# Optimization experiments

Hardware: AMD Instinct MI355X
Metric: run time of the kernel (lower is better)

Reference implementation:

```python
import jax, jax.numpy as jnp
import numpy as np

B, S, H = 4, 2048, 768
NUM_POS = B * (S // 4)  # fixed count of positive clc_label entries (2048, even)
NEG_BIG = -1000000000.0


def setup_inputs() -> dict:
    key = jax.random.key(0)
    k1, k2, k3, k4, k5 = jax.random.split(key, 5)
    encoded_states = jax.random.normal(k1, (B, S, H), dtype=jnp.float32)
    # sorted cell-ids -> contiguous segments for the equality mask
    indicator = jnp.sort(jax.random.randint(k2, (B, S), 0, 256, dtype=jnp.int32), axis=-1)
    # clc_label: first S//4 positions per row are positive targets (class ids in [1,S)),
    # last S//2 positions are -1 (attendable keys), rest 0 (ignored)
    pos_labels = jax.random.randint(k3, (B, S // 4), 1, S, dtype=jnp.int32)
    clc_label = jnp.zeros((B, S), dtype=jnp.int32)
    clc_label = clc_label.at[:, : S // 4].set(pos_labels)
    clc_label = clc_label.at[:, S // 2:].set(-1)
    # uniform_linear params (torch Linear: y = x @ W.T + b)
    W = jax.random.normal(k4, (H, H), dtype=jnp.float32) / np.sqrt(H)
    b = jax.random.normal(k5, (H,), dtype=jnp.float32) * 0.01
    return {"encoded_states": encoded_states, "W": W, "b": b,
            "indicator": indicator, "clc_label": clc_label}


def _ce(logits, labels):
    # mean cross entropy; all labels are > 0 here so ignore_index=0 never triggers
    logp = jax.nn.log_softmax(logits, axis=-1)
    return -jnp.take_along_axis(logp, labels[:, None], axis=1).mean()


def reference(encoded_states, W, b, indicator, clc_label):
    # indicator-equality mask matmul == within-segment sum (the segment-reduce emulation)
    seg_mask = (indicator[:, :, None] == indicator[:, None, :]).astype(encoded_states.dtype)  # [B,S,S]
    agg = jnp.einsum("bij,bjh->bih", seg_mask, encoded_states)  # [B,S,H]
    # Q and K use the SAME linear on the same input -> compute once
    proj = jnp.tanh(agg @ W.T + b)  # [B,S,H]
    scores = jnp.einsum("bih,bjh->bij", proj, proj)  # [B,S,S]
    # attend only to positions where clc_label < 0
    allow = (clc_label < 0)[:, None, :]  # [B,1,S]
    scores = scores + jnp.where(allow, 0.0, NEG_BIG).astype(scores.dtype)
    flat = scores.reshape(-1, S)          # [B*S, S]
    labels = clc_label.reshape(-1)        # [B*S]
    pos_idx = jnp.nonzero(labels > 0, size=NUM_POS)[0]  # row-major order == torch bool-indexing
    logits = flat[pos_idx]                # [NUM_POS, S]
    labs = labels[pos_idx]                # [NUM_POS]
    sep_logits, sep_labels = logits[0::2], labs[0::2]
    tok_logits, tok_labels = logits[1::2], labs[1::2]
    sep_loss = _ce(sep_logits, sep_labels)
    tok_loss = _ce(tok_logits, tok_labels)
    sep_correct = jnp.sum((jnp.argmax(sep_logits, axis=-1).astype(jnp.int32) == sep_labels).astype(jnp.float32))
    tok_correct = jnp.sum((jnp.argmax(tok_logits, axis=-1).astype(jnp.int32) == tok_labels).astype(jnp.float32))
    sep_count = jnp.asarray(sep_logits.shape[0] + 1e-6, dtype=jnp.float32)
    tok_count = jnp.asarray(tok_logits.shape[0] + 1e-6, dtype=jnp.float32)
    return ((sep_loss, sep_correct, sep_count), (tok_loss, tok_correct, tok_count))
```

## Files before the change

### kernel.cpp

```cpp
#include <hip/hip_runtime.h>
#include <math.h>
#include <limits.h>

#define BB 4
#define SS 2048
#define HH 768
#define MAXSEG 256
#define NUM_POS (BB*(SS/4))
#define NEG_BIG -1000000000.0f

typedef _Float16 f16x8 __attribute__((ext_vector_type(8)));
typedef _Float16 f16x4 __attribute__((ext_vector_type(4)));
typedef float    f32x4 __attribute__((ext_vector_type(4)));

__device__ __forceinline__ int blockExclScan(int v, int* sWave, int lane, int wid)
{
  int x = v;
  #pragma unroll
  for (int off = 1; off < 64; off <<= 1) {
    int y = __shfl_up(x, off, 64);
    if (lane >= off) x += y;
  }
  if (lane == 63) sWave[wid] = x;
  __syncthreads();
  int base = 0;
  for (int w = 0; w < wid; w++) base += sWave[w];
  return base + x - v;
}

__global__ __launch_bounds__(256) void k_scan(
    const int* __restrict__ ind, const int* __restrict__ clc,
    const float* __restrict__ W, _Float16* __restrict__ Wh,
    int* __restrict__ seg_id, int* __restrict__ seg_start,
    int* __restrict__ nseg, int* __restrict__ pos_cnt,
    int* __restrict__ allowCnt, int* __restrict__ firstAllow,
    int* __restrict__ posSegOff, int* __restrict__ posSeg,
    float* __restrict__ accum, int* __restrict__ counter)
{
  int t = threadIdx.x;
  if (blockIdx.x >= BB) {
    int idx = (blockIdx.x - BB)*256 + t;
    float4 v = ((const float4*)W)[idx];
    f16x4 h;
    h[0] = (_Float16)v.x; h[1] = (_Float16)v.y;
    h[2] = (_Float16)v.z; h[3] = (_Float16)v.w;
    *(f16x4*)(Wh + (size_t)idx*4) = h;
    return;
  }
  int b = blockIdx.x;
  int lane = t & 63, wid = t >> 6;
  __shared__ int sInd[SS];
  __shared__ int sWave[4];
  __shared__ int sAC[MAXSEG];
  __shared__ int sFA[MAXSEG];
  if (b == 0 && t < 4) accum[t] = 0.f;
  if (b == 0 && t == 4) *counter = 0;
  for (int i = t; i < SS; i += 256) sInd[i] = ind[b*SS + i];
  sAC[t] = 0; sFA[t] = INT_MAX;
  __syncthreads();

  int i0 = t * 8;
  int f[8], cv[8];
  int lsum = 0;
  #pragma unroll
  for (int u = 0; u < 8; u++) {
    int i = i0 + u;
    f[u] = (i == 0) ? 0 : (sInd[i] != sInd[i-1]);
    cv[u] = clc[b*SS + i];
    lsum += f[u];
  }
  int run = blockExclScan(lsum, sWave, lane, wid);
  int rid[8];
  #pragma unroll
  for (int u = 0; u < 8; u++) {
    int i = i0 + u;
    run += f[u];
    rid[u] = run;
    seg_id[b*SS + i] = run;
    if (f[u] || i == 0) seg_start[b*(MAXSEG+1) + run] = i;
  }
  if (t == 255) { nseg[b] = run + 1; seg_start[b*(MAXSEG+1) + run + 1] = SS; }

  #pragma unroll
  for (int u = 0; u < 8; u++) {
    if (cv[u] < 0) {
      atomicAdd(&sAC[rid[u]], 1);
      atomicMin(&sFA[rid[u]], i0 + u);
    }
  }
  __syncthreads();
  allowCnt[b*MAXSEG + t]   = sAC[t];
  firstAllow[b*MAXSEG + t] = sFA[t];
  __syncthreads();

  int p[8], kk[8];
  int psum = 0;
  #pragma unroll
  for (int u = 0; u < 8; u++) { p[u] = (cv[u] > 0) ? 1 : 0; psum += p[u]; }
  int rank = blockExclScan(psum, sWave, lane, wid);
  #pragma unroll
  for (int u = 0; u < 8; u++) {
    kk[u] = rank;
    if (p[u]) rank++;
  }
  if (t == 255) pos_cnt[b] = rank;
  __syncthreads();

  sAC[t] = 0;
  __syncthreads();
  #pragma unroll
  for (int u = 0; u < 8; u++) if (p[u]) atomicAdd(&sAC[rid[u]], 1);
  __syncthreads();
  int cnt = sAC[t];
  int off = blockExclScan(cnt, sWave, lane, wid);
  posSegOff[b*(MAXSEG+1) + t] = off;
  if (t == 255) posSegOff[b*(MAXSEG+1) + 256] = off + cnt;
  __syncthreads();
  sFA[t] = off;
  __syncthreads();
  #pragma unroll
  for (int u = 0; u < 8; u++) {
    if (p[u]) {
      int pos = atomicAdd(&sFA[rid[u]], 1);
      posSeg[b*SS + pos] = (kk[u] << 16) | (i0 + u);
    }
  }
}

__global__ __launch_bounds__(192) void k_segsum(
    const float* __restrict__ es, const int* __restrict__ seg_start,
    const int* __restrict__ nseg, _Float16* __restrict__ segsum_h)
{
  int blk = blockIdx.x, t = threadIdx.x;
  int b = blk >> 8, s = blk & 255;
  float4 acc = {0.f, 0.f, 0.f, 0.f};
  if (s < nseg[b]) {
    int st = seg_start[b*(MAXSEG+1) + s];
    int en = seg_start[b*(MAXSEG+1) + s + 1];
    const float* basep = es + (size_t)b*SS*HH + t*4;
    for (int i = st; i < en; i++) {
      float4 v = *(const float4*)(basep + (size_t)i*HH);
      acc.x += v.x; acc.y += v.y; acc.z += v.z; acc.w += v.w;
    }
  }
  f16x4 h;
  h[0] = (_Float16)acc.x; h[1] = (_Float16)acc.y;
  h[2] = (_Float16)acc.z; h[3] = (_Float16)acc.w;
  *(f16x4*)(segsum_h + ((size_t)b*MAXSEG + s)*HH + t*4) = h;
}

__global__ __launch_bounds__(256) void k_gemmU(
    const _Float16* __restrict__ Ah, const _Float16* __restrict__ Wh,
    const float* __restrict__ bias, _Float16* __restrict__ Uh)
{
  int tid = threadIdx.x;
  int w = tid >> 6, lane = tid & 63;
  int tile = blockIdx.x*4 + w;
  int tm = tile / 24, tn = tile % 24;
  int rb = tm*32, cb = tn*32;
  int m0 = lane & 15, quad = lane >> 4;
  const _Float16* A0 = Ah + (size_t)(rb + m0)*HH + quad*8;
  const _Float16* A1 = A0 + (size_t)16*HH;
  const _Float16* B0 = Wh + (size_t)(cb + m0)*HH + quad*8;
  const _Float16* B1 = B0 + (size_t)16*HH;
  f32x4 acc00 = {0.f,0.f,0.f,0.f}, acc01 = {0.f,0.f,0.f,0.f};
  f32x4 acc10 = {0.f,0.f,0.f,0.f}, acc11 = {0.f,0.f,0.f,0.f};
  #pragma unroll 4
  for (int k0 = 0; k0 < HH; k0 += 32) {
    f16x8 a0 = *(const f16x8*)(A0 + k0);
    f16x8 a1 = *(const f16x8*)(A1 + k0);
    f16x8 b0 = *(const f16x8*)(B0 + k0);
    f16x8 b1 = *(const f16x8*)(B1 + k0);
    acc00 = __builtin_amdgcn_mfma_f32_16x16x32_f16(a0, b0, acc00, 0, 0, 0);
    acc01 = __builtin_amdgcn_mfma_f32_16x16x32_f16(a0, b1, acc01, 0, 0, 0);
    acc10 = __builtin_amdgcn_mfma_f32_16x16x32_f16(a1, b0, acc10, 0, 0, 0);
    acc11 = __builtin_amdgcn_mfma_f32_16x16x32_f16(a1, b1, acc11, 0, 0, 0);
  }
  float bc0 = bias[cb + m0], bc1 = bias[cb + 16 + m0];
  int r0 = rb + quad*4;
  #pragma unroll
  for (int i = 0; i < 4; i++) {
    Uh[(size_t)(r0+i)*HH    + cb + m0]      = (_Float16)tanhf(acc00[i] + bc0);
    Uh[(size_t)(r0+i)*HH    + cb + 16 + m0] = (_Float16)tanhf(acc01[i] + bc1);
    Uh[(size_t)(r0+16+i)*HH + cb + m0]      = (_Float16)tanhf(acc10[i] + bc0);
    Uh[(size_t)(r0+16+i)*HH + cb + 16 + m0] = (_Float16)tanhf(acc11[i] + bc1);
  }
}

__global__ __launch_bounds__(256) void k_gram(
    const _Float16* __restrict__ Uh, float* __restrict__ G)
{
  int tid = threadIdx.x;
  int w = tid >> 6, lane = tid & 63;
  int tile = blockIdx.x*4 + w;
  int b = tile >> 8, rem = tile & 255;
  int rb = (rem >> 4)*16, cb = (rem & 15)*16;
  int m0 = lane & 15, quad = lane >> 4;
  const _Float16* Ub = Uh + (size_t)b*MAXSEG*HH;
  const _Float16* A0 = Ub + (size_t)(rb + m0)*HH + quad*8;
  const _Float16* B0 = Ub + (size_t)(cb + m0)*HH + quad*8;
  f32x4 acc = {0.f,0.f,0.f,0.f};
  #pragma unroll 4
  for (int k0 = 0; k0 < HH; k0 += 32) {
    f16x8 a  = *(const f16x8*)(A0 + k0);
    f16x8 bb = *(const f16x8*)(B0 + k0);
    acc = __builtin_amdgcn_mfma_f32_16x16x32_f16(a, bb, acc, 0, 0, 0);
  }
  float* Gb = G + (size_t)b*MAXSEG*MAXSEG;
  int r0 = rb + quad*4;
  #pragma unroll
  for (int i = 0; i < 4; i++)
    Gb[(size_t)(r0+i)*MAXSEG + cb + m0] = acc[i];
}

__global__ __launch_bounds__(256) void k_tail(
    const float* __restrict__ G, const int* __restrict__ seg_id,
    const int* __restrict__ clc, const int* __restrict__ nseg,
    const int* __restrict__ pos_cnt, const int* __restrict__ allowCnt,
    const int* __restrict__ firstAllow, const int* __restrict__ posSegOff,
    const int* __restrict__ posSeg,
    float* __restrict__ accum, int* __restrict__ counter,
    float* __restrict__ out)
{
  __shared__ float sP[4][4];
  int t = threadIdx.x;
  int lane = t & 63, wid = t >> 6;
  int row = blockIdx.x * 4 + wid;
  int b = row >> 8, si = row & 255;

  float l0 = 0.f, c0 = 0.f, l1 = 0.f, c1 = 0.f;
  if (si < nseg[b]) {
    const float* g = G + ((size_t)b*MAXSEG + si)*MAXSEG;
    const int* ac = allowCnt + b*MAXSEG;
    const int* fa = firstAllow + b*MAXSEG;
    float gv[4]; int av[4], fv[4];
    #pragma unroll
    for (int q = 0; q < 4; q++) {
      int s = lane + 64*q;
      gv[q] = g[s]; av[q] = ac[s]; fv[q] = fa[s];
    }
    float m = -INFINITY;
    #pragma unroll
    for (int q = 0; q < 4; q++) if (av[q] > 0) m = fmaxf(m, gv[q]);
    #pragma unroll
    for (int off = 32; off > 0; off >>= 1) m = fmaxf(m, __shfl_xor(m, off, 64));
    float s = 0.f;
    #pragma unroll
    for (int q = 0; q < 4; q++) if (av[q] > 0) s += (float)av[q] * expf(gv[q] - m);
    #pragma unroll
    for (int off = 32; off > 0; off >>= 1) s += __shfl_xor(s, off, 64);
    float bv = -INFINITY; int bi = INT_MAX;
    #pragma unroll
    for (int q = 0; q < 4; q++) {
      if (av[q] > 0 && (gv[q] > bv || (gv[q] == bv && fv[q] < bi))) { bv = gv[q]; bi = fv[q]; }
    }
    #pragma unroll
    for (int off = 32; off > 0; off >>= 1) {
      float ov = __shfl_xor(bv, off, 64);
      int   oi = __shfl_xor(bi, off, 64);
      if (ov > bv || (ov == bv && oi < bi)) { bv = ov; bi = oi; }
    }
    float lseV = m + logf(s);

    int base_b = 0;
    for (int bb2 = 0; bb2 < b; bb2++) base_b += pos_cnt[bb2];
    int st = posSegOff[b*(MAXSEG+1) + si];
    int en = posSegOff[b*(MAXSEG+1) + si + 1];
    for (int pp = st + lane; pp < en; pp += 64) {
      int e = posSeg[b*SS + pp];
      int i = e & 0xFFFF, k = e >> 16;
      int L = clc[b*SS + i];
      int sL = seg_id[b*SS + L];
      float vL = G[((size_t)b*MAXSEG + si)*MAXSEG + sL]
               + (clc[b*SS + L] < 0 ? 0.0f : NEG_BIG);
      float loss = lseV - vL;
      float corr = (bi == L) ? 1.0f : 0.0f;
      if ((base_b + k) & 1) { l1 += loss; c1 += corr; }
      else                  { l0 += loss; c0 += corr; }
    }
  }
  #pragma unroll
  for (int off = 32; off > 0; off >>= 1) {
    l0 += __shfl_down(l0, off, 64);
    c0 += __shfl_down(c0, off, 64);
    l1 += __shfl_down(l1, off, 64);
    c1 += __shfl_down(c1, off, 64);
  }
  if (lane == 0) { sP[wid][0] = l0; sP[wid][1] = c0; sP[wid][2] = l1; sP[wid][3] = c1; }
  __syncthreads();
  if (t == 0) {
    float v0 = sP[0][0]+sP[1][0]+sP[2][0]+sP[3][0];
    float v1 = sP[0][1]+sP[1][1]+sP[2][1]+sP[3][1];
    float v2 = sP[0][2]+sP[1][2]+sP[2][2]+sP[3][2];
    float v3 = sP[0][3]+sP[1][3]+sP[2][3]+sP[3][3];
    atomicAdd(&accum[0], v0);
    atomicAdd(&accum[1], v1);
    atomicAdd(&accum[2], v2);
    atomicAdd(&accum[3], v3);
    __threadfence();
    int old = atomicAdd(counter, 1);
    if (old == gridDim.x - 1) {
      float L0 = atomicAdd(&accum[0], 0.0f);
      float C0 = atomicAdd(&accum[1], 0.0f);
      float L1 = atomicAdd(&accum[2], 0.0f);
      float C1 = atomicAdd(&accum[3], 0.0f);
      float n = (float)(NUM_POS/2);
      out[0] = L0 / n;
      out[1] = C0;
      out[2] = n + 1e-6f;
      out[3] = L1 / n;
      out[4] = C1;
      out[5] = n + 1e-6f;
    }
  }
}

extern "C" void kernel_launch(void* const* d_in, const int* in_sizes, int n_in,
                              void* d_out, int out_size, void* d_ws, size_t ws_size,
                              hipStream_t stream)
{
  const float* es   = (const float*)d_in[0];
  const float* W    = (const float*)d_in[1];
  const float* bias = (const float*)d_in[2];
  const int*   ind  = (const int*)d_in[3];
  const int*   clc  = (const int*)d_in[4];
  float* out = (float*)d_out;

  char* ws = (char*)d_ws;
  float* accum      = (float*)(ws + 0);
  int*   counter    = (int*)(ws + 16);
  int*   nseg       = (int*)(ws + 256);
  int*   pos_cnt    = (int*)(ws + 512);
  int*   seg_start  = (int*)(ws + 1024);
  int*   seg_id     = (int*)(ws + 8192);
  int*   posSegOff  = (int*)(ws + 40960);
  int*   posSeg     = (int*)(ws + 49152);
  int*   allowCnt   = (int*)(ws + 81920);
  int*   firstAllow = (int*)(ws + 86016);
  _Float16* segsum_h = (_Float16*)(ws + 90112);
  _Float16* Wh       = (_Float16*)(ws + 1662976);
  _Float16* Uh       = (_Float16*)(ws + 2842624);
  float*    G        = (float*)(ws + 4415488);

  k_scan<<<BB + 576, 256, 0, stream>>>(ind, clc, W, Wh, seg_id, seg_start,
                                       nseg, pos_cnt, allowCnt, firstAllow,
                                       posSegOff, posSeg, accum, counter);
  k_segsum<<<BB*MAXSEG, 192, 0, stream>>>(es, seg_start, nseg, segsum_h);
  k_gemmU<<<192, 256, 0, stream>>>(segsum_h, Wh, bias, Uh);
  k_gram<<<256, 256, 0, stream>>>(Uh, G);
  k_tail<<<256, 256, 0, stream>>>(G, seg_id, clc, nseg, pos_cnt, allowCnt,
                                  firstAllow, posSegOff, posSeg,
                                  accum, counter, out);
}
```

Before: 132.4 us.

## Fuse segment-sum into scan kernel and gram matrix into tail kernel

The segment-sum work now runs inside the front kernel. Each segment block redoes the indicator boundary scan itself to find its own start and end, so it no longer waits on a separate scan launch. The gram-matrix computation moves into the tail kernel, which builds a 16-row slab of G in shared memory and consumes it directly. This removes two kernel launches and the global write and read of G. In exchange, the indicator scan is repeated by every segment block, and the fused tail runs only 64 blocks, which lowers parallelism in the gram phase.

```diff
diff --git a/kernel.cpp b/kernel.cpp
--- a/kernel.cpp
+++ b/kernel.cpp
@@ -8,6 +8,8 @@
 #define MAXSEG 256
 #define NUM_POS (BB*(SS/4))
 #define NEG_BIG -1000000000.0f
+#define NSEGSUM (BB*MAXSEG)
+#define NWCAST  576
 
 typedef _Float16 f16x8 __attribute__((ext_vector_type(8)));
 typedef _Float16 f16x4 __attribute__((ext_vector_type(4)));
@@ -28,18 +30,27 @@
   return base + x - v;
 }
 
-__global__ __launch_bounds__(256) void k_scan(
+__global__ __launch_bounds__(256) void k_front(
+    const float* __restrict__ es, const float* __restrict__ W,
     const int* __restrict__ ind, const int* __restrict__ clc,
-    const float* __restrict__ W, _Float16* __restrict__ Wh,
-    int* __restrict__ seg_id, int* __restrict__ seg_start,
-    int* __restrict__ nseg, int* __restrict__ pos_cnt,
+    _Float16* __restrict__ segsum_h, _Float16* __restrict__ Wh,
+    int* __restrict__ seg_id, int* __restrict__ pos_cnt,
     int* __restrict__ allowCnt, int* __restrict__ firstAllow,
     int* __restrict__ posSegOff, int* __restrict__ posSeg,
     float* __restrict__ accum, int* __restrict__ counter)
 {
   int t = threadIdx.x;
-  if (blockIdx.x >= BB) {
-    int idx = (blockIdx.x - BB)*256 + t;
+  int lane = t & 63, wid = t >> 6;
+  int blk = blockIdx.x;
+
+  __shared__ int sInd[SS];
+  __shared__ int sWave[4];
+  __shared__ int sAC[MAXSEG];
+  __shared__ int sFA[MAXSEG];
+  __shared__ int sStEn[2];
+
+  if (blk >= NSEGSUM + BB) {
+    int idx = (blk - NSEGSUM - BB)*256 + t;
     float4 v = ((const float4*)W)[idx];
     f16x4 h;
     h[0] = (_Float16)v.x; h[1] = (_Float16)v.y;
@@ -47,12 +58,48 @@
     *(f16x4*)(Wh + (size_t)idx*4) = h;
     return;
   }
-  int b = blockIdx.x;
-  int lane = t & 63, wid = t >> 6;
-  __shared__ int sInd[SS];
-  __shared__ int sWave[4];
-  __shared__ int sAC[MAXSEG];
-  __shared__ int sFA[MAXSEG];
+
+  if (blk < NSEGSUM) {
+    int b = blk >> 8, s = blk & 255;
+    for (int i = t; i < SS; i += 256) sInd[i] = ind[b*SS + i];
+    if (t == 0) { sStEn[0] = SS; sStEn[1] = SS; }
+    __syncthreads();
+    int i0 = t * 8;
+    int f[8]; int lsum = 0;
+    #pragma unroll
+    for (int u = 0; u < 8; u++) {
+      int i = i0 + u;
+      f[u] = (i == 0) ? 0 : (sInd[i] != sInd[i-1]);
+      lsum += f[u];
+    }
+    int run = blockExclScan(lsum, sWave, lane, wid);
+    #pragma unroll
+    for (int u = 0; u < 8; u++) {
+      int i = i0 + u;
+      run += f[u];
+      if (run == s   && (f[u] || i == 0)) sStEn[0] = i;
+      if (run == s+1 && f[u])             sStEn[1] = i;
+    }
+    __syncthreads();
+    int st = sStEn[0], en = sStEn[1];
+    float4 acc = {0.f, 0.f, 0.f, 0.f};
+    if (t < 192 && st < SS) {
+      const float* basep = es + (size_t)b*SS*HH + t*4;
+      for (int i = st; i < en; i++) {
+        float4 v = *(const float4*)(basep + (size_t)i*HH);
+        acc.x += v.x; acc.y += v.y; acc.z += v.z; acc.w += v.w;
+      }
+    }
+    if (t < 192) {
+      f16x4 h;
+      h[0] = (_Float16)acc.x; h[1] = (_Float16)acc.y;
+      h[2] = (_Float16)acc.z; h[3] = (_Float16)acc.w;
+      *(f16x4*)(segsum_h + ((size_t)b*MAXSEG + s)*HH + t*4) = h;
+    }
+    return;
+  }
+
+  int b = blk - NSEGSUM;
   if (b == 0 && t < 4) accum[t] = 0.f;
   if (b == 0 && t == 4) *counter = 0;
   for (int i = t; i < SS; i += 256) sInd[i] = ind[b*SS + i];
@@ -73,13 +120,10 @@
   int rid[8];
   #pragma unroll
   for (int u = 0; u < 8; u++) {
-    int i = i0 + u;
     run += f[u];
     rid[u] = run;
-    seg_id[b*SS + i] = run;
-    if (f[u] || i == 0) seg_start[b*(MAXSEG+1) + run] = i;
-  }
-  if (t == 255) { nseg[b] = run + 1; seg_start[b*(MAXSEG+1) + run + 1] = SS; }
+    seg_id[b*SS + i0 + u] = run;
+  }
 
   #pragma unroll
   for (int u = 0; u < 8; u++) {
@@ -125,28 +169,6 @@
       posSeg[b*SS + pos] = (kk[u] << 16) | (i0 + u);
     }
   }
-}
-
-__global__ __launch_bounds__(192) void k_segsum(
-    const float* __restrict__ es, const int* __restrict__ seg_start,
-    const int* __restrict__ nseg, _Float16* __restrict__ segsum_h)
-{
-  int blk = blockIdx.x, t = threadIdx.x;
-  int b = blk >> 8, s = blk & 255;
-  float4 acc = {0.f, 0.f, 0.f, 0.f};
-  if (s < nseg[b]) {
-    int st = seg_start[b*(MAXSEG+1) + s];
-    int en = seg_start[b*(MAXSEG+1) + s + 1];
-    const float* basep = es + (size_t)b*SS*HH + t*4;
-    for (int i = st; i < en; i++) {
-      float4 v = *(const float4*)(basep + (size_t)i*HH);
-      acc.x += v.x; acc.y += v.y; acc.z += v.z; acc.w += v.w;
-    }
-  }
-  f16x4 h;
-  h[0] = (_Float16)acc.x; h[1] = (_Float16)acc.y;
-  h[2] = (_Float16)acc.z; h[3] = (_Float16)acc.w;
-  *(f16x4*)(segsum_h + ((size_t)b*MAXSEG + s)*HH + t*4) = h;
 }
 
 __global__ __launch_bounds__(256) void k_gemmU(
@@ -187,57 +209,56 @@
   }
 }
 
-__global__ __launch_bounds__(256) void k_gram(
-    const _Float16* __restrict__ Uh, float* __restrict__ G)
-{
-  int tid = threadIdx.x;
-  int w = tid >> 6, lane = tid & 63;
-  int tile = blockIdx.x*4 + w;
-  int b = tile >> 8, rem = tile & 255;
-  int rb = (rem >> 4)*16, cb = (rem & 15)*16;
-  int m0 = lane & 15, quad = lane >> 4;
-  const _Float16* Ub = Uh + (size_t)b*MAXSEG*HH;
-  const _Float16* A0 = Ub + (size_t)(rb + m0)*HH + quad*8;
-  const _Float16* B0 = Ub + (size_t)(cb + m0)*HH + quad*8;
-  f32x4 acc = {0.f,0.f,0.f,0.f};
-  #pragma unroll 4
-  for (int k0 = 0; k0 < HH; k0 += 32) {
-    f16x8 a  = *(const f16x8*)(A0 + k0);
-    f16x8 bb = *(const f16x8*)(B0 + k0);
-    acc = __builtin_amdgcn_mfma_f32_16x16x32_f16(a, bb, acc, 0, 0, 0);
-  }
-  float* Gb = G + (size_t)b*MAXSEG*MAXSEG;
-  int r0 = rb + quad*4;
-  #pragma unroll
-  for (int i = 0; i < 4; i++)
-    Gb[(size_t)(r0+i)*MAXSEG + cb + m0] = acc[i];
-}
-
-__global__ __launch_bounds__(256) void k_tail(
-    const float* __restrict__ G, const int* __restrict__ seg_id,
-    const int* __restrict__ clc, const int* __restrict__ nseg,
-    const int* __restrict__ pos_cnt, const int* __restrict__ allowCnt,
-    const int* __restrict__ firstAllow, const int* __restrict__ posSegOff,
-    const int* __restrict__ posSeg,
+__global__ __launch_bounds__(256) void k_gramtail(
+    const _Float16* __restrict__ Uh, const int* __restrict__ seg_id,
+    const int* __restrict__ clc, const int* __restrict__ pos_cnt,
+    const int* __restrict__ allowCnt, const int* __restrict__ firstAllow,
+    const int* __restrict__ posSegOff, const int* __restrict__ posSeg,
     float* __restrict__ accum, int* __restrict__ counter,
     float* __restrict__ out)
 {
+  __shared__ float Gs[16][260];
   __shared__ float sP[4][4];
   int t = threadIdx.x;
   int lane = t & 63, wid = t >> 6;
-  int row = blockIdx.x * 4 + wid;
-  int b = row >> 8, si = row & 255;
-
+  int b = blockIdx.x >> 4;
+  int rb = (blockIdx.x & 15) * 16;
+  int m0 = lane & 15, quad = lane >> 4;
+  const _Float16* Ub = Uh + (size_t)b*MAXSEG*HH;
+  const _Float16* Ap = Ub + (size_t)(rb + m0)*HH + quad*8;
+
+  #pragma unroll
+  for (int ct = 0; ct < 4; ct++) {
+    int cb = (wid*4 + ct)*16;
+    const _Float16* Bp = Ub + (size_t)(cb + m0)*HH + quad*8;
+    f32x4 acc = {0.f,0.f,0.f,0.f};
+    #pragma unroll 4
+    for (int k0 = 0; k0 < HH; k0 += 32) {
+      f16x8 a  = *(const f16x8*)(Ap + k0);
+      f16x8 bb = *(const f16x8*)(Bp + k0);
+      acc = __builtin_amdgcn_mfma_f32_16x16x32_f16(a, bb, acc, 0, 0, 0);
+    }
+    #pragma unroll
+    for (int i = 0; i < 4; i++)
+      Gs[quad*4 + i][cb + m0] = acc[i];
+  }
+  __syncthreads();
+
+  const int* ac = allowCnt + b*MAXSEG;
+  const int* fa = firstAllow + b*MAXSEG;
+  int base_b = 0;
+  for (int x = 0; x < b; x++) base_b += pos_cnt[x];
   float l0 = 0.f, c0 = 0.f, l1 = 0.f, c1 = 0.f;
-  if (si < nseg[b]) {
-    const float* g = G + ((size_t)b*MAXSEG + si)*MAXSEG;
-    const int* ac = allowCnt + b*MAXSEG;
-    const int* fa = firstAllow + b*MAXSEG;
+
+  #pragma unroll
+  for (int q2 = 0; q2 < 4; q2++) {
+    int row = wid*4 + q2;
+    int si = rb + row;
     float gv[4]; int av[4], fv[4];
     #pragma unroll
     for (int q = 0; q < 4; q++) {
-      int s = lane + 64*q;
-      gv[q] = g[s]; av[q] = ac[s]; fv[q] = fa[s];
+      int s2 = lane + 64*q;
+      gv[q] = Gs[row][s2]; av[q] = ac[s2]; fv[q] = fa[s2];
     }
     float m = -INFINITY;
     #pragma unroll
@@ -262,8 +283,6 @@
     }
     float lseV = m + logf(s);
 
-    int base_b = 0;
-    for (int bb2 = 0; bb2 < b; bb2++) base_b += pos_cnt[bb2];
     int st = posSegOff[b*(MAXSEG+1) + si];
     int en = posSegOff[b*(MAXSEG+1) + si + 1];
     for (int pp = st + lane; pp < en; pp += 64) {
@@ -271,14 +290,14 @@
       int i = e & 0xFFFF, k = e >> 16;
       int L = clc[b*SS + i];
       int sL = seg_id[b*SS + L];
-      float vL = G[((size_t)b*MAXSEG + si)*MAXSEG + sL]
-               + (clc[b*SS + L] < 0 ? 0.0f : NEG_BIG);
+      float vL = Gs[row][sL] + (clc[b*SS + L] < 0 ? 0.0f : NEG_BIG);
       float loss = lseV - vL;
       float corr = (bi == L) ? 1.0f : 0.0f;
       if ((base_b + k) & 1) { l1 += loss; c1 += corr; }
       else                  { l0 += loss; c0 += corr; }
     }
   }
+
   #pragma unroll
   for (int off = 32; off > 0; off >>= 1) {
     l0 += __shfl_down(l0, off, 64);
@@ -289,17 +308,13 @@
   if (lane == 0) { sP[wid][0] = l0; sP[wid][1] = c0; sP[wid][2] = l1; sP[wid][3] = c1; }
   __syncthreads();
   if (t == 0) {
-    float v0 = sP[0][0]+sP[1][0]+sP[2][0]+sP[3][0];
-    float v1 = sP[0][1]+sP[1][1]+sP[2][1]+sP[3][1];
-    float v2 = sP[0][2]+sP[1][2]+sP[2][2]+sP[3][2];
-    float v3 = sP[0][3]+sP[1][3]+sP[2][3]+sP[3][3];
-    atomicAdd(&accum[0], v0);
-    atomicAdd(&accum[1], v1);
-    atomicAdd(&accum[2], v2);
-    atomicAdd(&accum[3], v3);
+    atomicAdd(&accum[0], sP[0][0]+sP[1][0]+sP[2][0]+sP[3][0]);
+    atomicAdd(&accum[1], sP[0][1]+sP[1][1]+sP[2][1]+sP[3][1]);
+    atomicAdd(&accum[2], sP[0][2]+sP[1][2]+sP[2][2]+sP[3][2]);
+    atomicAdd(&accum[3], sP[0][3]+sP[1][3]+sP[2][3]+sP[3][3]);
     __threadfence();
     int old = atomicAdd(counter, 1);
-    if (old == gridDim.x - 1) {
+    if (old == (int)gridDim.x - 1) {
       float L0 = atomicAdd(&accum[0], 0.0f);
       float C0 = atomicAdd(&accum[1], 0.0f);
       float L1 = atomicAdd(&accum[2], 0.0f);
@@ -329,9 +344,7 @@
   char* ws = (char*)d_ws;
   float* accum      = (float*)(ws + 0);
   int*   counter    = (int*)(ws + 16);
-  int*   nseg       = (int*)(ws + 256);
   int*   pos_cnt    = (int*)(ws + 512);
-  int*   seg_start  = (int*)(ws + 1024);
   int*   seg_id     = (int*)(ws + 8192);
   int*   posSegOff  = (int*)(ws + 40960);
   int*   posSeg     = (int*)(ws + 49152);
@@ -340,15 +353,12 @@
   _Float16* segsum_h = (_Float16*)(ws + 90112);
   _Float16* Wh       = (_Float16*)(ws + 1662976);
   _Float16* Uh       = (_Float16*)(ws + 2842624);
-  float*    G        = (float*)(ws + 4415488);
-
-  k_scan<<<BB + 576, 256, 0, stream>>>(ind, clc, W, Wh, seg_id, seg_start,
-                                       nseg, pos_cnt, allowCnt, firstAllow,
-                                       posSegOff, posSeg, accum, counter);
-  k_segsum<<<BB*MAXSEG, 192, 0, stream>>>(es, seg_start, nseg, segsum_h);
+
+  k_front<<<NSEGSUM + BB + NWCAST, 256, 0, stream>>>(
+      es, W, ind, clc, segsum_h, Wh, seg_id, pos_cnt,
+      allowCnt, firstAllow, posSegOff, posSeg, accum, counter);
   k_gemmU<<<192, 256, 0, stream>>>(segsum_h, Wh, bias, Uh);
-  k_gram<<<256, 256, 0, stream>>>(Uh, G);
-  k_tail<<<256, 256, 0, stream>>>(G, seg_id, clc, nseg, pos_cnt, allowCnt,
-                                  firstAllow, posSegOff, posSeg,
-                                  accum, counter, out);
-}
+  k_gramtail<<<64, 256, 0, stream>>>(Uh, seg_id, clc, pos_cnt, allowCnt,
+                                     firstAllow, posSegOff, posSeg,
+                                     accum, counter, out);
+}
```

Result: slower. 137.1 us (+3.5%).
